# Optimization experiments

Hardware: AMD Instinct MI355X
Metric: run time of the kernel (lower is better)

The kernel has to match this reference:

```python
import jax, jax.numpy as jnp
import numpy as np
import math

EMBED_DIM = 1024
N_HEADS = 16
HEAD_DIM = EMBED_DIM // N_HEADS
B, N = 2, 2048


def setup_inputs() -> dict:
    key = jax.random.key(0)
    k1, k2, k3 = jax.random.split(key, 3)
    x = jax.random.normal(k1, (B, N, EMBED_DIM), dtype=jnp.float32)
    # Per-head Linear(D, 3*head_dim), stacked over heads. PyTorch Linear init scale ~1/sqrt(fan_in).
    bound = 1.0 / math.sqrt(EMBED_DIM)
    Wkqv = jax.random.uniform(k2, (N_HEADS, EMBED_DIM, 3 * HEAD_DIM), dtype=jnp.float32, minval=-bound, maxval=bound)
    bkqv = jax.random.uniform(k3, (N_HEADS, 3 * HEAD_DIM), dtype=jnp.float32, minval=-bound, maxval=bound)
    return {"x": x, "Wkqv": Wkqv, "bkqv": bkqv}


def reference(x, Wkqv, bkqv):
    Bx, Nx, D = x.shape
    hd = Wkqv.shape[-1] // 3
    # all heads at once: [B, H, N, 3*hd]
    proj = jnp.einsum('bnd,hdf->bhnf', x, Wkqv) + bkqv[None, :, None, :]
    # torch.split order in the original is (k, q, v)
    k, q, v = jnp.split(proj, 3, axis=-1)
    # scores = q @ k^T / sqrt(head_dim)   [B, H, N, N]
    scores = jnp.einsum('bhqd,bhkd->bhqk', q, k) / math.sqrt(hd)
    causal = jnp.tril(jnp.ones((Nx, Nx), dtype=bool))
    scores = jnp.where(causal[None, None, :, :], scores, -jnp.inf)
    attn = jax.nn.softmax(scores, axis=-1)
    out = jnp.einsum('bhqk,bhkd->bhqd', attn, v)  # [B, H, N, hd]
    # concat heads -> [B, N, D]  (forward() passes no out_matrix, so no output projection)
    return out.transpose(0, 2, 1, 3).reshape(Bx, Nx, D)
```

## Files before the change

### kernel.cpp

```cpp
#include <hip/hip_runtime.h>
#include <math.h>

typedef float f32x4 __attribute__((ext_vector_type(4)));
typedef __bf16 bf16x8 __attribute__((ext_vector_type(8)));
typedef __bf16 bf16x4 __attribute__((ext_vector_type(4)));

#define MFMA16(a, b, c) __builtin_amdgcn_mfma_f32_16x16x32_bf16((a), (b), (c), 0, 0, 0)

constexpr int Bsz = 2, Nseq = 2048, Dm = 1024, Hh = 16, HDim = 64, F3 = 192;
constexpr int Mrows = Bsz * Nseq;
constexpr int NC = Hh * F3;
constexpr float QSCALE = 0.125f * 1.4426950408889634f;

__device__ inline void load_lds16(const void* g, void* l) {
    __builtin_amdgcn_global_load_lds((const __attribute__((address_space(1))) void*)g,
                                     (__attribute__((address_space(3))) void*)l, 16, 0, 0);
}

#define FENCE asm volatile("" ::: "memory")
#define BARRIER do { FENCE; __builtin_amdgcn_s_barrier(); FENCE; } while (0)


__global__ __launch_bounds__(256) void conv_xw_kernel(const float* __restrict__ x,
                                                      __bf16* __restrict__ xb,
                                                      const float* __restrict__ w,
                                                      __bf16* __restrict__ wt) {
    __shared__ __bf16 tile[32][66];
    if (blockIdx.x < 2048) {
        int i = blockIdx.x * 256 + threadIdx.x;
        const float4* xv = reinterpret_cast<const float4*>(x);
        float4 a = xv[2 * i];
        float4 b = xv[2 * i + 1];
        bf16x8 o = {(__bf16)a.x, (__bf16)a.y, (__bf16)a.z, (__bf16)a.w,
                    (__bf16)b.x, (__bf16)b.y, (__bf16)b.z, (__bf16)b.w};
        *reinterpret_cast<bf16x8*>(xb + 8 * i) = o;
    } else {
        int id = blockIdx.x - 2048;
        int h = id / 96, rem = id % 96;
        int d0 = (rem & 31) * 32, c0 = (rem >> 5) * 64;
        for (int i = threadIdx.x; i < 32 * 64; i += 256) {
            int di = i >> 6, cj = i & 63;
            tile[di][cj] = (__bf16)w[(size_t)(h * Dm + d0 + di) * F3 + c0 + cj];
        }
        __syncthreads();
        for (int i = threadIdx.x; i < 32 * 64; i += 256) {
            int ci = i >> 5, dj = i & 31;
            wt[(size_t)(h * F3 + c0 + ci) * Dm + d0 + dj] = tile[dj][ci];
        }
    }
}

__global__ __launch_bounds__(256) void conv_w_kernel(const float* __restrict__ w,
                                                     __bf16* __restrict__ wt) {
    __shared__ __bf16 tile[32][66];
    int h = blockIdx.z, d0 = blockIdx.x * 32, c0 = blockIdx.y * 64;
    for (int i = threadIdx.x; i < 32 * 64; i += 256) {
        int di = i >> 6, cj = i & 63;
        tile[di][cj] = (__bf16)w[(size_t)(h * Dm + d0 + di) * F3 + c0 + cj];
    }
    __syncthreads();
    for (int i = threadIdx.x; i < 32 * 64; i += 256) {
        int ci = i >> 5, dj = i & 31;
        wt[(size_t)(h * F3 + c0 + ci) * Dm + d0 + dj] = tile[dj][ci];
    }
}

__global__ __launch_bounds__(512, 4) void gemm_proj(const __bf16* __restrict__ xb,
                                                    const __bf16* __restrict__ wt,
                                                    const float* __restrict__ bias,
                                                    __bf16* __restrict__ kbuf,
                                                    __bf16* __restrict__ qbuf,
                                                    __bf16* __restrict__ vt) {
    __shared__ __align__(16) __bf16 Ab[2][128 * 64];
    __shared__ __align__(16) __bf16 Bb[2][192 * 64];

    int flat = blockIdx.x;
    int swz = (flat & 7) * 64 + (flat >> 3);
    int bm = swz >> 4, bn = swz & 15;
    int r0 = bm * 128, n0 = bn * 192;

    int w = threadIdx.x >> 6, lane = threadIdx.x & 63;
    int col = lane & 15, quad = lane >> 4;
    int wm = w >> 2, wn = w & 3;

    f32x4 acc[4][3] = {};

    int rl = lane >> 3;
    int cg = ((lane & 7) ^ rl) * 8;

    auto stage = [&](int t, int s) {
#pragma unroll
        for (int i = 0; i < 2; i++) {
            int rowb = w * 16 + i * 8;
            load_lds16(xb + (size_t)(r0 + rowb + rl) * Dm + t * 64 + cg,
                       &Ab[s][rowb * 64]);
        }
#pragma unroll
        for (int i = 0; i < 3; i++) {
            int rowb = w * 24 + i * 8;
            load_lds16(wt + (size_t)(n0 + rowb + rl) * Dm + t * 64 + cg,
                       &Bb[s][rowb * 64]);
        }
    };

    stage(0, 0);
    stage(1, 1);

    for (int j = 0; j < 16; j++) {
        int s = j & 1;
        if (j < 15) asm volatile("s_waitcnt vmcnt(5)" ::: "memory");
        else        asm volatile("s_waitcnt vmcnt(0)" ::: "memory");
        BARRIER;

#pragma unroll
        for (int ks = 0; ks < 2; ks++) {
            int cq = ks * 4 + quad;
            bf16x8 af[4], bfr[3];
#pragma unroll
            for (int mt = 0; mt < 4; mt++) {
                int row = wm * 64 + mt * 16 + col;
                af[mt] = *reinterpret_cast<const bf16x8*>(
                    &Ab[s][row * 64 + ((cq ^ (row & 7)) * 8)]);
            }
#pragma unroll
            for (int nt = 0; nt < 3; nt++) {
                int row = wn * 48 + nt * 16 + col;
                bfr[nt] = *reinterpret_cast<const bf16x8*>(
                    &Bb[s][row * 64 + ((cq ^ (row & 7)) * 8)]);
            }
            __builtin_amdgcn_s_setprio(1);
#pragma unroll
            for (int mt = 0; mt < 4; mt++)
#pragma unroll
                for (int nt = 0; nt < 3; nt++)
                    acc[mt][nt] = MFMA16(af[mt], bfr[nt], acc[mt][nt]);
            __builtin_amdgcn_s_setprio(0);
        }

        BARRIER;
        if (j + 2 < 16) stage(j + 2, s);
    }

#pragma unroll
    for (int nt = 0; nt < 3; nt++) {
        int g = n0 + wn * 48 + nt * 16 + col;
        int h = g / F3, c = g - h * F3;
        float bv = bias[g];
        bool isq = (c >= 64 && c < 128), isv = (c >= 128);
        int cd = c & 63;
#pragma unroll
        for (int mt = 0; mt < 4; mt++) {
#pragma unroll
            for (int rg = 0; rg < 4; rg++) {
                int r = r0 + wm * 64 + mt * 16 + quad * 4 + rg;
                int b = r >> 11, n = r & (Nseq - 1);
                float v = acc[mt][nt][rg] + bv;
                if (isq) v *= QSCALE;
                size_t bh = (size_t)(b * Hh + h);
                if (isv) {
                    int np = (n & ~63) | (((n >> 5) & 1) << 5) | ((n & 12) << 1)
                           | (((n >> 4) & 1) << 2) | (n & 3);
                    vt[(bh * HDim + cd) * Nseq + np] = (__bf16)v;
                } else {
                    ((isq) ? qbuf : kbuf)[(bh * Nseq + n) * HDim + cd] = (__bf16)v;
                }
            }
        }
    }
}

__global__ __launch_bounds__(256) void proj_small(const float* __restrict__ x,
                                                  const __bf16* __restrict__ wt,
                                                  const float* __restrict__ bias,
                                                  __bf16* __restrict__ kbuf,
                                                  __bf16* __restrict__ qbuf,
                                                  __bf16* __restrict__ vt) {
    int h = blockIdx.y;
    int wave = threadIdx.x >> 6, lane = threadIdx.x & 63;
    int col = lane & 15, quad = lane >> 4;
    int r0 = blockIdx.x * 128 + wave * 32;

    f32x4 acc[12][2] = {};
    const float* xr0 = x + (size_t)(r0 + col) * Dm + quad * 8;
    const float* xr1 = xr0 + 16 * Dm;
    const __bf16* wbase = wt + (size_t)(h * F3 + col) * Dm + quad * 8;

    for (int k0 = 0; k0 < Dm; k0 += 32) {
        float4 a0lo = *reinterpret_cast<const float4*>(xr0 + k0);
        float4 a0hi = *reinterpret_cast<const float4*>(xr0 + k0 + 4);
        float4 a1lo = *reinterpret_cast<const float4*>(xr1 + k0);
        float4 a1hi = *reinterpret_cast<const float4*>(xr1 + k0 + 4);
        bf16x8 a0 = {(__bf16)a0lo.x, (__bf16)a0lo.y, (__bf16)a0lo.z, (__bf16)a0lo.w,
                     (__bf16)a0hi.x, (__bf16)a0hi.y, (__bf16)a0hi.z, (__bf16)a0hi.w};
        bf16x8 a1 = {(__bf16)a1lo.x, (__bf16)a1lo.y, (__bf16)a1lo.z, (__bf16)a1lo.w,
                     (__bf16)a1hi.x, (__bf16)a1hi.y, (__bf16)a1hi.z, (__bf16)a1hi.w};
#pragma unroll
        for (int ct = 0; ct < 12; ct++) {
            bf16x8 bf = *reinterpret_cast<const bf16x8*>(wbase + ct * 16 * Dm + k0);
            acc[ct][0] = MFMA16(a0, bf, acc[ct][0]);
            acc[ct][1] = MFMA16(a1, bf, acc[ct][1]);
        }
    }
#pragma unroll
    for (int ct = 0; ct < 12; ct++) {
        int c = ct * 16 + col;
        float bv = bias[h * F3 + c];
        int cd = c & 63;
        bool isq = (c >= 64 && c < 128), isv = (c >= 128);
#pragma unroll
        for (int rt = 0; rt < 2; rt++) {
#pragma unroll
            for (int rg = 0; rg < 4; rg++) {
                int r = r0 + rt * 16 + quad * 4 + rg;
                int b = r >> 11, n = r & (Nseq - 1);
                float v = acc[ct][rt][rg] + bv;
                if (isq) v *= QSCALE;
                size_t bh = (size_t)(b * Hh + h);
                if (isv) {
                    int np = (n & ~63) | (((n >> 5) & 1) << 5) | ((n & 12) << 1)
                           | (((n >> 4) & 1) << 2) | (n & 3);
                    vt[(bh * HDim + cd) * Nseq + np] = (__bf16)v;
                } else {
                    ((isq) ? qbuf : kbuf)[(bh * Nseq + n) * HDim + cd] = (__bf16)v;
                }
            }
        }
    }
}

__global__ __launch_bounds__(256) void attn_kernel(const __bf16* __restrict__ qbuf,
                                                   const __bf16* __restrict__ kbuf,
                                                   const __bf16* __restrict__ vt,
                                                   float* __restrict__ out) {
    __shared__ __align__(16) __bf16 Kb[2][64 * 64];
    __shared__ __align__(16) __bf16 Vb[2][64 * 64];
    int bh = blockIdx.x;
    int b = bh >> 4, h = bh & 15;
    int tile = 31 - blockIdx.y;
    int wave = threadIdx.x >> 6, lane = threadIdx.x & 63;
    int col = lane & 15, quad = lane >> 4;
    int q0 = tile * 64 + wave * 16;

    const __bf16* qbase = qbuf + (size_t)bh * Nseq * HDim;
    const __bf16* kbase = kbuf + (size_t)bh * Nseq * HDim;
    const __bf16* vbase = vt + (size_t)bh * HDim * Nseq;

    bf16x8 aq0 = *reinterpret_cast<const bf16x8*>(qbase + (q0 + col) * HDim + quad * 8);
    bf16x8 aq1 = *reinterpret_cast<const bf16x8*>(qbase + (q0 + col) * HDim + quad * 8 + 32);

    const bf16x8 vone = {(__bf16)1.f, (__bf16)1.f, (__bf16)1.f, (__bf16)1.f,
                         (__bf16)1.f, (__bf16)1.f, (__bf16)1.f, (__bf16)1.f};

    f32x4 o[4] = {};
    f32x4 ls = {};

    int mb = tile * 64;
    int loop_end = mb + 64;
    int qi = q0 + col;

    int rl = lane >> 3;
    int srow0 = wave * 16 + rl;
    int srow1 = wave * 16 + 8 + rl;
    int sc = (lane & 7) ^ rl;
    const __bf16* ksrc0 = kbase + srow0 * HDim + sc * 8;
    const __bf16* ksrc1 = kbase + srow1 * HDim + sc * 8;
    const __bf16* vsrc0 = vbase + (size_t)srow0 * Nseq + sc * 8;
    const __bf16* vsrc1 = vbase + (size_t)srow1 * Nseq + sc * 8;
    int d0 = wave * 1024, d1 = wave * 1024 + 512;

    int sw0 = ((quad ^ (col & 7)) * 8);
    int sw1 = (((quad + 4) ^ (col & 7)) * 8);

    load_lds16(ksrc0, &Kb[0][d0]);
    load_lds16(ksrc1, &Kb[0][d1]);
    load_lds16(vsrc0, &Vb[0][d0]);
    load_lds16(vsrc1, &Vb[0][d1]);
    FENCE;

    int s = 0;
    for (int kb = 0; kb < loop_end; kb += 64) {
        asm volatile("s_waitcnt vmcnt(0)" ::: "memory");
        BARRIER;
        int nkb = kb + 64;
        load_lds16(ksrc0 + nkb * HDim, &Kb[s ^ 1][d0]);
        load_lds16(ksrc1 + nkb * HDim, &Kb[s ^ 1][d1]);
        load_lds16(vsrc0 + nkb, &Vb[s ^ 1][d0]);
        load_lds16(vsrc1 + nkb, &Vb[s ^ 1][d1]);

        bool masked = (kb == mb);
        const __bf16* Kcur = Kb[s];
        const __bf16* Vcur = Vb[s];
        f32x4 z = {};
        f32x4 sc4[4];
#pragma unroll
        for (int g = 0; g < 4; g++) {
            const __bf16* krow = Kcur + (col + 16 * g) * 64;
            bf16x8 k0 = *reinterpret_cast<const bf16x8*>(krow + sw0);
            bf16x8 k1 = *reinterpret_cast<const bf16x8*>(krow + sw1);
            sc4[g] = MFMA16(k0, aq0, z);
            sc4[g] = MFMA16(k1, aq1, sc4[g]);
        }
        bf16x8 pa0, pa1;
        if (masked) {
#pragma unroll
            for (int g = 0; g < 4; g++)
#pragma unroll
                for (int r = 0; r < 4; r++) {
                    int key = kb + 16 * g + quad * 4 + r;
                    float p = (key <= qi) ? exp2f(sc4[g][r]) : 0.f;
                    if (g < 2) pa0[(g & 1) * 4 + r] = (__bf16)p;
                    else       pa1[(g & 1) * 4 + r] = (__bf16)p;
                }
        } else {
#pragma unroll
            for (int g = 0; g < 4; g++)
#pragma unroll
                for (int r = 0; r < 4; r++) {
                    float p = exp2f(sc4[g][r]);
                    if (g < 2) pa0[(g & 1) * 4 + r] = (__bf16)p;
                    else       pa1[(g & 1) * 4 + r] = (__bf16)p;
                }
        }
        ls = MFMA16(pa0, vone, ls);
        ls = MFMA16(pa1, vone, ls);
#pragma unroll
        for (int nt = 0; nt < 4; nt++) {
            const __bf16* vrow = Vcur + (col + 16 * nt) * 64;
            bf16x8 v0 = *reinterpret_cast<const bf16x8*>(vrow + sw0);
            bf16x8 v1 = *reinterpret_cast<const bf16x8*>(vrow + sw1);
            o[nt] = MFMA16(pa0, v0, o[nt]);
            o[nt] = MFMA16(pa1, v1, o[nt]);
        }
        s ^= 1;
    }

    float linv[4];
#pragma unroll
    for (int r = 0; r < 4; r++) linv[r] = 1.f / ls[r];
#pragma unroll
    for (int nt = 0; nt < 4; nt++) {
#pragma unroll
        for (int r = 0; r < 4; r++) {
            int qr = q0 + quad * 4 + r;
            out[((size_t)(b * Nseq + qr)) * Dm + h * HDim + nt * 16 + col] = o[nt][r] * linv[r];
        }
    }
}

extern "C" void kernel_launch(void* const* d_in, const int* in_sizes, int n_in,
                              void* d_out, int out_size, void* d_ws, size_t ws_size,
                              hipStream_t stream) {
    const float* x = nullptr;
    const float* w = nullptr;
    const float* bias = nullptr;
    for (int i = 0; i < n_in; i++) {
        if (in_sizes[i] == Mrows * Dm) x = (const float*)d_in[i];
        else if (in_sizes[i] == Hh * Dm * F3) w = (const float*)d_in[i];
        else if (in_sizes[i] == Hh * F3) bias = (const float*)d_in[i];
    }
    float* outp = (float*)d_out;

    char* ws = (char*)d_ws;
    __bf16* wt = (__bf16*)(ws);
    __bf16* kbuf = (__bf16*)(ws + 6291456);
    __bf16* qbuf = (__bf16*)(ws + 6291456 + 8388608);
    __bf16* vt = (__bf16*)(ws + 6291456 + 2 * 8388608);
    __bf16* xb = (__bf16*)(ws + 6291456 + 3 * 8388608);

    if (ws_size >= (size_t)(6291456 + 4 * 8388608)) {
        conv_xw_kernel<<<3584, 256, 0, stream>>>(x, xb, w, wt);
        gemm_proj<<<dim3((Mrows / 128) * (NC / 192)), 512, 0, stream>>>(xb, wt, bias, kbuf, qbuf, vt);
    } else {
        conv_w_kernel<<<dim3(Dm / 32, F3 / 64, Hh), 256, 0, stream>>>(w, wt);
        proj_small<<<dim3(Mrows / 128, Hh), 256, 0, stream>>>(x, wt, bias, kbuf, qbuf, vt);
    }
    attn_kernel<<<dim3(32, 32), 256, 0, stream>>>(qbuf, kbuf, vt, outp);
}
```

Baseline: 145.3 us.

## Single-buffer attention LDS for higher occupancy and vectorize V-transpose stores

```diff
diff --git a/kernel.cpp b/kernel.cpp
--- a/kernel.cpp
+++ b/kernel.cpp
@@ -150,19 +150,23 @@
         int cd = c & 63;
 #pragma unroll
         for (int mt = 0; mt < 4; mt++) {
-#pragma unroll
-            for (int rg = 0; rg < 4; rg++) {
-                int r = r0 + wm * 64 + mt * 16 + quad * 4 + rg;
-                int b = r >> 11, n = r & (Nseq - 1);
-                float v = acc[mt][nt][rg] + bv;
-                if (isq) v *= QSCALE;
-                size_t bh = (size_t)(b * Hh + h);
-                if (isv) {
-                    int np = (n & ~63) | (((n >> 5) & 1) << 5) | ((n & 12) << 1)
-                           | (((n >> 4) & 1) << 2) | (n & 3);
-                    vt[(bh * HDim + cd) * Nseq + np] = (__bf16)v;
-                } else {
-                    ((isq) ? qbuf : kbuf)[(bh * Nseq + n) * HDim + cd] = (__bf16)v;
+            int rbase = r0 + wm * 64 + mt * 16 + quad * 4;
+            int b = rbase >> 11, n = rbase & (Nseq - 1);
+            size_t bh = (size_t)(b * Hh + h);
+            if (isv) {
+                int npb = (n & ~63) | (((n >> 5) & 1) << 5) | ((n & 12) << 1)
+                        | (((n >> 4) & 1) << 2);
+                bf16x4 pv;
+#pragma unroll
+                for (int rg = 0; rg < 4; rg++) pv[rg] = (__bf16)(acc[mt][nt][rg] + bv);
+                *reinterpret_cast<bf16x4*>(&vt[(bh * HDim + cd) * Nseq + npb]) = pv;
+            } else {
+                __bf16* dst = (isq) ? qbuf : kbuf;
+#pragma unroll
+                for (int rg = 0; rg < 4; rg++) {
+                    float v = acc[mt][nt][rg] + bv;
+                    if (isq) v *= QSCALE;
+                    dst[(bh * Nseq + n + rg) * HDim + cd] = (__bf16)v;
                 }
             }
         }
@@ -228,12 +232,12 @@
     }
 }
 
-__global__ __launch_bounds__(256) void attn_kernel(const __bf16* __restrict__ qbuf,
-                                                   const __bf16* __restrict__ kbuf,
-                                                   const __bf16* __restrict__ vt,
-                                                   float* __restrict__ out) {
-    __shared__ __align__(16) __bf16 Kb[2][64 * 64];
-    __shared__ __align__(16) __bf16 Vb[2][64 * 64];
+__global__ __launch_bounds__(256, 8) void attn_kernel(const __bf16* __restrict__ qbuf,
+                                                      const __bf16* __restrict__ kbuf,
+                                                      const __bf16* __restrict__ vt,
+                                                      float* __restrict__ out) {
+    __shared__ __align__(16) __bf16 Kb[64 * 64];
+    __shared__ __align__(16) __bf16 Vb[64 * 64];
     int bh = blockIdx.x;
     int b = bh >> 4, h = bh & 15;
     int tile = 31 - blockIdx.y;
@@ -271,30 +275,21 @@
     int sw0 = ((quad ^ (col & 7)) * 8);
     int sw1 = (((quad + 4) ^ (col & 7)) * 8);
 
-    load_lds16(ksrc0, &Kb[0][d0]);
-    load_lds16(ksrc1, &Kb[0][d1]);
-    load_lds16(vsrc0, &Vb[0][d0]);
-    load_lds16(vsrc1, &Vb[0][d1]);
-    FENCE;
-
-    int s = 0;
     for (int kb = 0; kb < loop_end; kb += 64) {
+        BARRIER;
+        load_lds16(ksrc0 + kb * HDim, &Kb[d0]);
+        load_lds16(ksrc1 + kb * HDim, &Kb[d1]);
+        load_lds16(vsrc0 + kb, &Vb[d0]);
+        load_lds16(vsrc1 + kb, &Vb[d1]);
         asm volatile("s_waitcnt vmcnt(0)" ::: "memory");
         BARRIER;
-        int nkb = kb + 64;
-        load_lds16(ksrc0 + nkb * HDim, &Kb[s ^ 1][d0]);
-        load_lds16(ksrc1 + nkb * HDim, &Kb[s ^ 1][d1]);
-        load_lds16(vsrc0 + nkb, &Vb[s ^ 1][d0]);
-        load_lds16(vsrc1 + nkb, &Vb[s ^ 1][d1]);
 
         bool masked = (kb == mb);
-        const __bf16* Kcur = Kb[s];
-        const __bf16* Vcur = Vb[s];
         f32x4 z = {};
         f32x4 sc4[4];
 #pragma unroll
         for (int g = 0; g < 4; g++) {
-            const __bf16* krow = Kcur + (col + 16 * g) * 64;
+            const __bf16* krow = Kb + (col + 16 * g) * 64;
             bf16x8 k0 = *reinterpret_cast<const bf16x8*>(krow + sw0);
             bf16x8 k1 = *reinterpret_cast<const bf16x8*>(krow + sw1);
             sc4[g] = MFMA16(k0, aq0, z);
@@ -325,13 +320,12 @@
         ls = MFMA16(pa1, vone, ls);
 #pragma unroll
         for (int nt = 0; nt < 4; nt++) {
-            const __bf16* vrow = Vcur + (col + 16 * nt) * 64;
+            const __bf16* vrow = Vb + (col + 16 * nt) * 64;
             bf16x8 v0 = *reinterpret_cast<const bf16x8*>(vrow + sw0);
             bf16x8 v1 = *reinterpret_cast<const bf16x8*>(vrow + sw1);
             o[nt] = MFMA16(pa0, v0, o[nt]);
             o[nt] = MFMA16(pa1, v1, o[nt]);
         }
-        s ^= 1;
     }
 
     float linv[4];
```

Result: slower. 240.5 us (+65.5%).
